# Optimization experiments

Measured on AMD Instinct MI355X. Metric: run time of the kernel, lower is better.

Reference implementation:

```python
import jax, jax.numpy as jnp
import numpy as np

B, T, C = 8, 512, 1024
H, E = 16, 64          # n_head, head_dim; H*E == C
L = 2048               # cached (prefix) length in the KV cache


def setup_inputs() -> dict:
    key = jax.random.key(0)
    ks = jax.random.split(key, 6)
    scale = 0.02
    return {
        "x": jax.random.normal(ks[0], (B, T, C), jnp.float32),
        "k_cache": jax.random.normal(ks[1], (B, H, L, E), jnp.float32),
        "v_cache": jax.random.normal(ks[2], (B, H, L, E), jnp.float32),
        "Wqkv": jax.random.normal(ks[3], (C, 3 * C), jnp.float32) * scale,
        "bqkv": jnp.zeros((3 * C,), jnp.float32),
        "Wproj": jax.random.normal(ks[4], (C, C), jnp.float32) * scale,
        "bproj": jnp.zeros((C,), jnp.float32),
    }


def reference(x, k_cache, v_cache, Wqkv, bqkv, Wproj, bproj):
    qkv = x @ Wqkv + bqkv
    q, k, v = jnp.split(qkv, 3, axis=-1)

    def to_heads(t):
        return t.reshape(B, T, H, E).transpose(0, 2, 1, 3)

    q, k, v = to_heads(q), to_heads(k), to_heads(v)

    # append new k,v to the cache (kv_cache.update + get)
    k_full = jnp.concatenate([k_cache, k], axis=2)  # (B,H,L+T,E)
    v_full = jnp.concatenate([v_cache, v], axis=2)

    # manual self-attention with cache-offset causal mask: row i (global pos L+i)
    # may attend to cols j <= L+i  (bias[L:L+T, :L+T])
    att = jnp.einsum("bhte,bhse->bhts", q, k_full) * (1.0 / np.sqrt(E))
    i = jnp.arange(T)[:, None] + L
    j = jnp.arange(L + T)[None, :]
    att = jnp.where(j <= i, att, -jnp.inf)
    att = jax.nn.softmax(att, axis=-1)

    y = jnp.einsum("bhts,bhse->bhte", att, v_full)
    y = y.transpose(0, 2, 1, 3).reshape(B, T, C)
    return y @ Wproj + bproj
```

## Files before the change

### kernel.cpp

```cpp
#include <hip/hip_runtime.h>
#include <hip/hip_bf16.h>

typedef unsigned short u16;
typedef unsigned int u32;

constexpr int B_ = 8, T_ = 512, C_ = 1024, H_ = 16, E_ = 64, L_ = 2048;
constexpr int S_ = L_ + T_;

typedef __bf16 bf16x8 __attribute__((ext_vector_type(8)));
typedef float f32x4 __attribute__((ext_vector_type(4)));

#define QSCALE 0.18033688011112042f

__device__ inline u16 f2bf(float f) {
  u32 u = __float_as_uint(f);
  u32 r = (u + 0x7fffu + ((u >> 16) & 1u)) >> 16;
  return (u16)r;
}

__device__ inline u32 pk2(float a, float b) {
  union { __hip_bfloat162 h; u32 u; } cv;
  cv.h = __float22bfloat162_rn(float2{a, b});
  return cv.u;
}

__device__ inline void gload_lds16(const u16* g, u16* l) {
  __builtin_amdgcn_global_load_lds(
      (const __attribute__((address_space(1))) u32*)g,
      (__attribute__((address_space(3))) u32*)l, 16, 0, 0);
}

__global__ __launch_bounds__(256) void convert_f32_bf16(const float* __restrict__ in,
                                                        u16* __restrict__ out) {
  const int i = blockIdx.x * 256 + threadIdx.x;
  const float4 a0 = ((const float4*)in)[i * 2];
  const float4 a1 = ((const float4*)in)[i * 2 + 1];
  uint4 p;
  p.x = pk2(a0.x, a0.y);
  p.y = pk2(a0.z, a0.w);
  p.z = pk2(a1.x, a1.y);
  p.w = pk2(a1.z, a1.w);
  ((uint4*)out)[i] = p;
}

__global__ __launch_bounds__(256) void transpose_f32_bf16(const float* __restrict__ in,
                                                          u16* __restrict__ out,
                                                          int R, int Ccols) {
  __shared__ u16 tile[64][65];
  const int r0 = blockIdx.y * 64;
  const int c0 = blockIdx.x * 64;
  const int tr = threadIdx.x >> 6;
  const int tc = threadIdx.x & 63;
#pragma unroll
  for (int i = 0; i < 16; ++i)
    tile[tr + i * 4][tc] = f2bf(in[(size_t)(r0 + tr + i * 4) * Ccols + c0 + tc]);
  __syncthreads();
#pragma unroll
  for (int i = 0; i < 16; ++i)
    out[(size_t)(c0 + tr + i * 4) * R + r0 + tc] = tile[tc][tr + i * 4];
}

__global__ __launch_bounds__(256) void prep_kv(const float* __restrict__ kc,
                                               const float* __restrict__ vc,
                                               u16* __restrict__ Km,
                                               u16* __restrict__ Vtm) {
  __shared__ u16 vt[64 * 72];
  const int s0 = (blockIdx.x & 31) * 64;
  const int bh = blockIdx.x >> 5;
  const int tid = threadIdx.x;
  const int srow = tid >> 2;
  const int eq = (tid & 3) * 16;

  {
    const float* kp = kc + ((size_t)bh * L_ + s0 + srow) * E_ + eq;
    float kv[16];
    *(float4*)(kv + 0) = *(const float4*)(kp + 0);
    *(float4*)(kv + 4) = *(const float4*)(kp + 4);
    *(float4*)(kv + 8) = *(const float4*)(kp + 8);
    *(float4*)(kv + 12) = *(const float4*)(kp + 12);
    uint4 p0, p1;
    p0.x = pk2(kv[0], kv[1]);
    p0.y = pk2(kv[2], kv[3]);
    p0.z = pk2(kv[4], kv[5]);
    p0.w = pk2(kv[6], kv[7]);
    p1.x = pk2(kv[8], kv[9]);
    p1.y = pk2(kv[10], kv[11]);
    p1.z = pk2(kv[12], kv[13]);
    p1.w = pk2(kv[14], kv[15]);
    u16* kd = Km + ((size_t)bh * S_ + s0 + srow) * E_ + eq;
    *(uint4*)kd = p0;
    *(uint4*)(kd + 8) = p1;
  }
  {
    const float* vp = vc + ((size_t)bh * L_ + s0 + srow) * E_ + eq;
    float vv[16];
    *(float4*)(vv + 0) = *(const float4*)(vp + 0);
    *(float4*)(vv + 4) = *(const float4*)(vp + 4);
    *(float4*)(vv + 8) = *(const float4*)(vp + 8);
    *(float4*)(vv + 12) = *(const float4*)(vp + 12);
    uint4 p0, p1;
    p0.x = pk2(vv[0], vv[1]);
    p0.y = pk2(vv[2], vv[3]);
    p0.z = pk2(vv[4], vv[5]);
    p0.w = pk2(vv[6], vv[7]);
    p1.x = pk2(vv[8], vv[9]);
    p1.y = pk2(vv[10], vv[11]);
    p1.z = pk2(vv[12], vv[13]);
    p1.w = pk2(vv[14], vv[15]);
    *(uint4*)(vt + srow * 72 + eq) = p0;
    *(uint4*)(vt + srow * 72 + eq + 8) = p1;
  }
  __syncthreads();
  {
    const int erow = tid >> 2;
    const int sq = (tid & 3) * 16;
    u16 o[16];
#pragma unroll
    for (int j = 0; j < 16; ++j) o[j] = vt[(sq + j) * 72 + erow];
    u16* vd = Vtm + ((size_t)bh * E_ + erow) * S_ + s0 + sq;
    *(uint4*)vd = *(uint4*)(o + 0);
    *(uint4*)(vd + 8) = *(uint4*)(o + 8);
  }
}

template <int MODE>
__global__ __launch_bounds__(256) void gemm128(const u16* __restrict__ A,
                                               const u16* __restrict__ BT,
                                               const float* __restrict__ bias,
                                               u16* __restrict__ qh,
                                               u16* __restrict__ Km,
                                               u16* __restrict__ Vtm,
                                               float* __restrict__ outf,
                                               int M, int N, int K) {
  __shared__ __align__(16) u16 As[128 * 32];
  __shared__ __align__(16) u16 Bs[128 * 32];
  const int tid = threadIdx.x;
  const int lane = tid & 63;
  const int w = tid >> 6;
  const int m0 = blockIdx.y * 128;
  const int n0 = blockIdx.x * 128;
  const int wm = (w >> 1) * 64;
  const int wn = (w & 1) * 64;
  const int fm = lane & 15;
  const int fk = (lane >> 4) * 8;

  const int srow = w * 16 + (lane >> 2);
  const int scol = (lane & 3) * 8;
  const u16* Ag = A + (size_t)(m0 + srow) * K + scol;
  const u16* Bg = BT + (size_t)(n0 + srow) * K + scol;
  u16* AsU = As + w * 512;
  u16* BsU = Bs + w * 512;

  f32x4 acc[4][4];
#pragma unroll
  for (int i = 0; i < 4; ++i)
#pragma unroll
    for (int j = 0; j < 4; ++j) acc[i][j] = f32x4{0.f, 0.f, 0.f, 0.f};

  for (int k0 = 0; k0 < K; k0 += 32) {
    gload_lds16(Ag, AsU);
    gload_lds16(Ag + (size_t)64 * K, AsU + 2048);
    gload_lds16(Bg, BsU);
    gload_lds16(Bg + (size_t)64 * K, BsU + 2048);
    Ag += 32;
    Bg += 32;
    __syncthreads();
    bf16x8 af[4], bf[4];
#pragma unroll
    for (int i = 0; i < 4; ++i)
      af[i] = *(const bf16x8*)(As + (wm + i * 16 + fm) * 32 + fk);
#pragma unroll
    for (int j = 0; j < 4; ++j)
      bf[j] = *(const bf16x8*)(Bs + (wn + j * 16 + fm) * 32 + fk);
#pragma unroll
    for (int i = 0; i < 4; ++i)
#pragma unroll
      for (int j = 0; j < 4; ++j)
        acc[i][j] = __builtin_amdgcn_mfma_f32_16x16x32_bf16(af[i], bf[j], acc[i][j], 0, 0, 0);
    __syncthreads();
  }

  const int rbase = (lane >> 4) * 4;
  const int cbase = lane & 15;
#pragma unroll
  for (int i = 0; i < 4; ++i)
#pragma unroll
    for (int j = 0; j < 4; ++j) {
      const int n = n0 + wn + j * 16 + cbase;
      const float bv = bias[n];
#pragma unroll
      for (int r = 0; r < 4; ++r) {
        const int m = m0 + wm + i * 16 + rbase + r;
        const float v = acc[i][j][r] + bv;
        if (MODE == 0) {
          const int seg = n >> 10;
          const int c = n & 1023;
          const int e = c & 63;
          const int bhh = ((m >> 9) * H_) + (c >> 6);
          const int t = m & 511;
          if (seg == 0)
            qh[((size_t)bhh * T_ + t) * E_ + e] = f2bf(v * QSCALE);
          else if (seg == 1)
            Km[((size_t)bhh * S_ + L_ + t) * E_ + e] = f2bf(v);
          else
            Vtm[((size_t)bhh * E_ + e) * S_ + L_ + t] = f2bf(v);
        } else {
          outf[(size_t)m * N + n] = v;
        }
      }
    }
}

__global__ __launch_bounds__(256) void attn_v3(const u16* __restrict__ qh,
                                               const u16* __restrict__ Km,
                                               const u16* __restrict__ Vtm,
                                               u16* __restrict__ y2) {
  __shared__ __align__(16) u16 Ks[64 * 72];
  __shared__ __align__(16) u16 Vts[64 * 72];
  __shared__ __align__(16) u16 Ps[4][32 * 72];

  const int tid = threadIdx.x;
  const int lane = tid & 63;
  const int w = tid >> 6;
  const int bh = blockIdx.x & 127;
  const int qt = blockIdx.x >> 7;
  const int h = bh & (H_ - 1);
  const int b = bh >> 4;
  const int t0 = qt * 128;

  const int col = lane & 15;
  const int fk = (lane >> 4) * 8;
  const int rbase = (lane >> 4) * 4;

  const u16* qbase = qh + ((size_t)bh * T_ + t0 + w * 32) * E_;
  bf16x8 qf[2][2];
#pragma unroll
  for (int q2 = 0; q2 < 2; ++q2)
#pragma unroll
    for (int ks = 0; ks < 2; ++ks)
      qf[q2][ks] = *(const bf16x8*)(qbase + (q2 * 16 + col) * E_ + ks * 32 + fk);

  const int srow = tid >> 2;
  const int sc8 = (tid & 3) * 16;

  f32x4 Yt[2][4];
  f32x4 lf[2];
#pragma unroll
  for (int q2 = 0; q2 < 2; ++q2) {
    lf[q2] = f32x4{0.f, 0.f, 0.f, 0.f};
#pragma unroll
    for (int et = 0; et < 4; ++et) Yt[q2][et] = f32x4{0.f, 0.f, 0.f, 0.f};
  }

  const bf16x8 ones = {(__bf16)1.f, (__bf16)1.f, (__bf16)1.f, (__bf16)1.f,
                       (__bf16)1.f, (__bf16)1.f, (__bf16)1.f, (__bf16)1.f};

  const int qmin_w = L_ + t0 + w * 32;
  const int nchunk = (L_ + t0 + 128) >> 6;
  const u16* KgB = Km + (size_t)bh * S_ * E_;
  const u16* VgB = Vtm + (size_t)bh * E_ * S_;

  for (int c0 = 0; c0 < nchunk; ++c0) {
    const int sbase = c0 << 6;
    __syncthreads();
    {
      const u16* kg = KgB + (size_t)(sbase + srow) * E_ + sc8;
      *(uint4*)(Ks + srow * 72 + sc8) = *(const uint4*)kg;
      *(uint4*)(Ks + srow * 72 + sc8 + 8) = *(const uint4*)(kg + 8);
      const u16* vg = VgB + (size_t)srow * S_ + sbase + sc8;
      *(uint4*)(Vts + srow * 72 + sc8) = *(const uint4*)vg;
      *(uint4*)(Vts + srow * 72 + sc8 + 8) = *(const uint4*)(vg + 8);
    }
    __syncthreads();

    if (sbase > qmin_w + 31) continue;

    f32x4 s[2][4];
#pragma unroll
    for (int kt = 0; kt < 4; ++kt) {
      const bf16x8 kb0 = *(const bf16x8*)(Ks + (kt * 16 + col) * 72 + fk);
      const bf16x8 kb1 = *(const bf16x8*)(Ks + (kt * 16 + col) * 72 + 32 + fk);
#pragma unroll
      for (int q2 = 0; q2 < 2; ++q2) {
        f32x4 z = {0.f, 0.f, 0.f, 0.f};
        z = __builtin_amdgcn_mfma_f32_16x16x32_bf16(qf[q2][0], kb0, z, 0, 0, 0);
        z = __builtin_amdgcn_mfma_f32_16x16x32_bf16(qf[q2][1], kb1, z, 0, 0, 0);
        s[q2][kt] = z;
      }
    }

    if (sbase + 63 > qmin_w) {
#pragma unroll
      for (int q2 = 0; q2 < 2; ++q2) {
        const int bound = qmin_w + q2 * 16 + rbase;
#pragma unroll
        for (int kt = 0; kt < 4; ++kt) {
          const int keypos = sbase + kt * 16 + col;
#pragma unroll
          for (int r = 0; r < 4; ++r)
            if (keypos > bound + r) s[q2][kt][r] = -1e30f;
        }
      }
    }

#pragma unroll
    for (int q2 = 0; q2 < 2; ++q2)
#pragma unroll
      for (int kt = 0; kt < 4; ++kt)
#pragma unroll
        for (int r = 0; r < 4; ++r) s[q2][kt][r] = exp2f(s[q2][kt][r]);

    u16* psw = Ps[w];
#pragma unroll
    for (int q2 = 0; q2 < 2; ++q2)
#pragma unroll
      for (int kt = 0; kt < 4; ++kt) {
        const u32 p01 = pk2(s[q2][kt][0], s[q2][kt][1]);
        const u32 p23 = pk2(s[q2][kt][2], s[q2][kt][3]);
        const int a = (q2 * 16 + rbase) * 72 + kt * 16 + col;
        psw[a] = (u16)p01;
        psw[a + 72] = (u16)(p01 >> 16);
        psw[a + 144] = (u16)p23;
        psw[a + 216] = (u16)(p23 >> 16);
      }

    bf16x8 pa[2][2];
#pragma unroll
    for (int q2 = 0; q2 < 2; ++q2)
#pragma unroll
      for (int ks = 0; ks < 2; ++ks)
        pa[q2][ks] = *(const bf16x8*)(psw + (q2 * 16 + col) * 72 + ks * 32 + fk);

#pragma unroll
    for (int q2 = 0; q2 < 2; ++q2) {
      lf[q2] = __builtin_amdgcn_mfma_f32_16x16x32_bf16(ones, pa[q2][0], lf[q2], 0, 0, 0);
      lf[q2] = __builtin_amdgcn_mfma_f32_16x16x32_bf16(ones, pa[q2][1], lf[q2], 0, 0, 0);
    }

#pragma unroll
    for (int et = 0; et < 4; ++et) {
      const bf16x8 vb0 = *(const bf16x8*)(Vts + (et * 16 + col) * 72 + fk);
      const bf16x8 vb1 = *(const bf16x8*)(Vts + (et * 16 + col) * 72 + 32 + fk);
#pragma unroll
      for (int q2 = 0; q2 < 2; ++q2) {
        Yt[q2][et] = __builtin_amdgcn_mfma_f32_16x16x32_bf16(vb0, pa[q2][0], Yt[q2][et], 0, 0, 0);
        Yt[q2][et] = __builtin_amdgcn_mfma_f32_16x16x32_bf16(vb1, pa[q2][1], Yt[q2][et], 0, 0, 0);
      }
    }
  }

#pragma unroll
  for (int q2 = 0; q2 < 2; ++q2) {
    const float rl = 1.f / lf[q2][0];
    const int t_out = t0 + w * 32 + q2 * 16 + col;
    u16* yp = y2 + ((size_t)b * T_ + t_out) * C_ + h * E_ + rbase;
#pragma unroll
    for (int et = 0; et < 4; ++et) {
      uint2 v;
      v.x = pk2(Yt[q2][et][0] * rl, Yt[q2][et][1] * rl);
      v.y = pk2(Yt[q2][et][2] * rl, Yt[q2][et][3] * rl);
      *(uint2*)(yp + et * 16) = v;
    }
  }
}

extern "C" void kernel_launch(void* const* d_in, const int* in_sizes, int n_in,
                              void* d_out, int out_size, void* d_ws, size_t ws_size,
                              hipStream_t stream) {
  const float* x = (const float*)d_in[0];
  const float* kc = (const float*)d_in[1];
  const float* vc = (const float*)d_in[2];
  const float* Wqkv = (const float*)d_in[3];
  const float* bqkv = (const float*)d_in[4];
  const float* Wproj = (const float*)d_in[5];
  const float* bproj = (const float*)d_in[6];
  float* out = (float*)d_out;

  u16* qh = (u16*)d_ws;
  u16* y2 = qh + 4194304;
  u16* xb = y2 + 4194304;
  u16* WqT = xb + 4194304;
  u16* WpT = WqT + 3145728;
  u16* Km = WpT + 1048576;
  u16* Vtm = Km + 20971520;

  convert_f32_bf16<<<dim3(2048), 256, 0, stream>>>(x, xb);
  transpose_f32_bf16<<<dim3(48, 16), 256, 0, stream>>>(Wqkv, WqT, 1024, 3072);
  transpose_f32_bf16<<<dim3(16, 16), 256, 0, stream>>>(Wproj, WpT, 1024, 1024);
  prep_kv<<<dim3(128 * 32), 256, 0, stream>>>(kc, vc, Km, Vtm);

  gemm128<0><<<dim3(24, 32), 256, 0, stream>>>(xb, WqT, bqkv, qh, Km, Vtm, nullptr,
                                               4096, 3072, 1024);

  attn_v3<<<dim3(512), 256, 0, stream>>>(qh, Km, Vtm, y2);

  gemm128<1><<<dim3(8, 32), 256, 0, stream>>>(y2, WpT, bproj, nullptr, nullptr,
                                              nullptr, out, 4096, 1024, 1024);
}
```

Before: 356.0 us.

## Rewrite attention with 32x32 MFMA, register P via permlane, double-buffered swizzled LDS

The attention kernel now uses 32x32x16 bf16 MFMA tiles, computing S^T so the softmax probabilities can be repacked into the PV operand in registers with v_permlane32_swap. This removes the per-wave P round trip through LDS. K/V tiles are double-buffered, with global loads for the next chunk issued into registers before compute, and stored into an XOR-swizzled unpadded LDS layout. Launch bounds now request 2 blocks per CU. The risks are higher register pressure from the f32x16 accumulators and correctness depending on the permlane layout.

```diff
diff --git a/kernel.cpp b/kernel.cpp
--- a/kernel.cpp
+++ b/kernel.cpp
@@ -9,6 +9,7 @@
 
 typedef __bf16 bf16x8 __attribute__((ext_vector_type(8)));
 typedef float f32x4 __attribute__((ext_vector_type(4)));
+typedef float f32x16 __attribute__((ext_vector_type(16)));
 
 #define QSCALE 0.18033688011112042f
 
@@ -22,6 +23,10 @@
   union { __hip_bfloat162 h; u32 u; } cv;
   cv.h = __float22bfloat162_rn(float2{a, b});
   return cv.u;
+}
+
+__device__ inline void pl32swap(u32& a, u32& b) {
+  asm("v_permlane32_swap_b32 %0, %1" : "+v"(a), "+v"(b));
 }
 
 __device__ inline void gload_lds16(const u16* g, u16* l) {
@@ -211,13 +216,12 @@
     }
 }
 
-__global__ __launch_bounds__(256) void attn_v3(const u16* __restrict__ qh,
-                                               const u16* __restrict__ Km,
-                                               const u16* __restrict__ Vtm,
-                                               u16* __restrict__ y2) {
-  __shared__ __align__(16) u16 Ks[64 * 72];
-  __shared__ __align__(16) u16 Vts[64 * 72];
-  __shared__ __align__(16) u16 Ps[4][32 * 72];
+__global__ __launch_bounds__(256, 2) void attn_v4(const u16* __restrict__ qh,
+                                                  const u16* __restrict__ Km,
+                                                  const u16* __restrict__ Vtm,
+                                                  u16* __restrict__ y2) {
+  __shared__ __align__(16) u16 Ks[2][64 * 64];
+  __shared__ __align__(16) u16 Vts[2][64 * 64];
 
   const int tid = threadIdx.x;
   const int lane = tid & 63;
@@ -228,28 +232,29 @@
   const int b = bh >> 4;
   const int t0 = qt * 128;
 
-  const int col = lane & 15;
-  const int fk = (lane >> 4) * 8;
-  const int rbase = (lane >> 4) * 4;
-
-  const u16* qbase = qh + ((size_t)bh * T_ + t0 + w * 32) * E_;
-  bf16x8 qf[2][2];
-#pragma unroll
-  for (int q2 = 0; q2 < 2; ++q2)
-#pragma unroll
-    for (int ks = 0; ks < 2; ++ks)
-      qf[q2][ks] = *(const bf16x8*)(qbase + (q2 * 16 + col) * E_ + ks * 32 + fk);
+  const int ln = lane & 31;
+  const int hi = lane >> 5;
+  const int swz = ln & 7;
+
+  const u16* qbase = qh + ((size_t)bh * T_ + t0 + w * 32 + ln) * E_;
+  bf16x8 qf[4];
+#pragma unroll
+  for (int et = 0; et < 4; ++et)
+    qf[et] = *(const bf16x8*)(qbase + et * 16 + hi * 8);
 
   const int srow = tid >> 2;
-  const int sc8 = (tid & 3) * 16;
-
-  f32x4 Yt[2][4];
-  f32x4 lf[2];
-#pragma unroll
-  for (int q2 = 0; q2 < 2; ++q2) {
-    lf[q2] = f32x4{0.f, 0.f, 0.f, 0.f};
-#pragma unroll
-    for (int et = 0; et < 4; ++et) Yt[q2][et] = f32x4{0.f, 0.f, 0.f, 0.f};
+  const int su = (tid & 3) * 2;
+  const u16* kg = Km + ((size_t)bh * S_ + srow) * E_ + su * 8;
+  const u16* vg = Vtm + ((size_t)bh * E_ + srow) * S_ + su * 8;
+  const int st0 = srow * 64 + ((su ^ (srow & 7)) * 8);
+  const int st1 = srow * 64 + (((su + 1) ^ (srow & 7)) * 8);
+
+  f32x16 Yt[2], lacc;
+#pragma unroll
+  for (int i = 0; i < 16; ++i) {
+    Yt[0][i] = 0.f;
+    Yt[1][i] = 0.f;
+    lacc[i] = 0.f;
   }
 
   const bf16x8 ones = {(__bf16)1.f, (__bf16)1.f, (__bf16)1.f, (__bf16)1.f,
@@ -257,111 +262,117 @@
 
   const int qmin_w = L_ + t0 + w * 32;
   const int nchunk = (L_ + t0 + 128) >> 6;
-  const u16* KgB = Km + (size_t)bh * S_ * E_;
-  const u16* VgB = Vtm + (size_t)bh * E_ * S_;
-
-  for (int c0 = 0; c0 < nchunk; ++c0) {
-    const int sbase = c0 << 6;
-    __syncthreads();
-    {
-      const u16* kg = KgB + (size_t)(sbase + srow) * E_ + sc8;
-      *(uint4*)(Ks + srow * 72 + sc8) = *(const uint4*)kg;
-      *(uint4*)(Ks + srow * 72 + sc8 + 8) = *(const uint4*)(kg + 8);
-      const u16* vg = VgB + (size_t)srow * S_ + sbase + sc8;
-      *(uint4*)(Vts + srow * 72 + sc8) = *(const uint4*)vg;
-      *(uint4*)(Vts + srow * 72 + sc8 + 8) = *(const uint4*)(vg + 8);
+
+  uint4 kr0 = *(const uint4*)(kg);
+  uint4 kr1 = *(const uint4*)(kg + 8);
+  uint4 vr0 = *(const uint4*)(vg);
+  uint4 vr1 = *(const uint4*)(vg + 8);
+  {
+    u16* kd = Ks[0];
+    u16* vd = Vts[0];
+    *(uint4*)(kd + st0) = kr0;
+    *(uint4*)(kd + st1) = kr1;
+    *(uint4*)(vd + st0) = vr0;
+    *(uint4*)(vd + st1) = vr1;
+  }
+  __syncthreads();
+
+  for (int c = 0; c < nchunk; ++c) {
+    const int sbase = c << 6;
+    const u16* ks = Ks[c & 1];
+    const u16* vs = Vts[c & 1];
+    const bool more = (c + 1 < nchunk);
+
+    if (more) {
+      const size_t ko = (size_t)(c + 1) * 64 * E_;
+      const int vo = (c + 1) * 64;
+      kr0 = *(const uint4*)(kg + ko);
+      kr1 = *(const uint4*)(kg + ko + 8);
+      vr0 = *(const uint4*)(vg + vo);
+      vr1 = *(const uint4*)(vg + vo + 8);
+    }
+
+    if (sbase <= qmin_w + 31) {
+      bf16x8 pa[4];
+#pragma unroll
+      for (int kb = 0; kb < 2; ++kb) {
+        f32x16 s;
+#pragma unroll
+        for (int i = 0; i < 16; ++i) s[i] = 0.f;
+#pragma unroll
+        for (int et = 0; et < 4; ++et) {
+          const bf16x8 kf = *(const bf16x8*)(
+              ks + (kb * 32 + ln) * 64 + (((et * 2 + hi) ^ swz) * 8));
+          s = __builtin_amdgcn_mfma_f32_32x32x16_bf16(kf, qf[et], s, 0, 0, 0);
+        }
+
+        if (sbase + 63 > qmin_w) {
+          const int qpos = qmin_w + ln;
+          const int kb0 = sbase + kb * 32 + hi * 4;
+#pragma unroll
+          for (int r = 0; r < 16; ++r) {
+            const int keypos = kb0 + (r & 3) + 8 * (r >> 2);
+            if (keypos > qpos) s[r] = -1e30f;
+          }
+        }
+
+#pragma unroll
+        for (int r = 0; r < 16; ++r) s[r] = exp2f(s[r]);
+
+#pragma unroll
+        for (int t = 0; t < 2; ++t) {
+          u32 x0 = pk2(s[8 * t + 0], s[8 * t + 1]);
+          u32 y0 = pk2(s[8 * t + 4], s[8 * t + 5]);
+          u32 x1 = pk2(s[8 * t + 2], s[8 * t + 3]);
+          u32 y1 = pk2(s[8 * t + 6], s[8 * t + 7]);
+          pl32swap(x0, y0);
+          pl32swap(x1, y1);
+          union { u32 u[4]; bf16x8 v; } pu;
+          pu.u[0] = x0;
+          pu.u[1] = x1;
+          pu.u[2] = y0;
+          pu.u[3] = y1;
+          pa[kb * 2 + t] = pu.v;
+        }
+      }
+
+#pragma unroll
+      for (int t = 0; t < 4; ++t)
+        lacc = __builtin_amdgcn_mfma_f32_32x32x16_bf16(ones, pa[t], lacc, 0, 0, 0);
+
+#pragma unroll
+      for (int eb = 0; eb < 2; ++eb)
+#pragma unroll
+        for (int t = 0; t < 4; ++t) {
+          const bf16x8 vf = *(const bf16x8*)(
+              vs + (eb * 32 + ln) * 64 + (((t * 2 + hi) ^ swz) * 8));
+          Yt[eb] = __builtin_amdgcn_mfma_f32_32x32x16_bf16(vf, pa[t], Yt[eb], 0, 0, 0);
+        }
+    }
+
+    if (more) {
+      u16* kd = Ks[(c + 1) & 1];
+      u16* vd = Vts[(c + 1) & 1];
+      *(uint4*)(kd + st0) = kr0;
+      *(uint4*)(kd + st1) = kr1;
+      *(uint4*)(vd + st0) = vr0;
+      *(uint4*)(vd + st1) = vr1;
     }
     __syncthreads();
-
-    if (sbase > qmin_w + 31) continue;
-
-    f32x4 s[2][4];
-#pragma unroll
-    for (int kt = 0; kt < 4; ++kt) {
-      const bf16x8 kb0 = *(const bf16x8*)(Ks + (kt * 16 + col) * 72 + fk);
-      const bf16x8 kb1 = *(const bf16x8*)(Ks + (kt * 16 + col) * 72 + 32 + fk);
-#pragma unroll
-      for (int q2 = 0; q2 < 2; ++q2) {
-        f32x4 z = {0.f, 0.f, 0.f, 0.f};
-        z = __builtin_amdgcn_mfma_f32_16x16x32_bf16(qf[q2][0], kb0, z, 0, 0, 0);
-        z = __builtin_amdgcn_mfma_f32_16x16x32_bf16(qf[q2][1], kb1, z, 0, 0, 0);
-        s[q2][kt] = z;
-      }
+  }
+
+  const float rl = 1.f / lacc[0];
+  const int t_out = t0 + w * 32 + ln;
+  u16* yp = y2 + ((size_t)b * T_ + t_out) * C_ + h * E_ + hi * 4;
+#pragma unroll
+  for (int eb = 0; eb < 2; ++eb)
+#pragma unroll
+    for (int g = 0; g < 4; ++g) {
+      uint2 st;
+      st.x = pk2(Yt[eb][4 * g + 0] * rl, Yt[eb][4 * g + 1] * rl);
+      st.y = pk2(Yt[eb][4 * g + 2] * rl, Yt[eb][4 * g + 3] * rl);
+      *(uint2*)(yp + eb * 32 + g * 8) = st;
     }
-
-    if (sbase + 63 > qmin_w) {
-#pragma unroll
-      for (int q2 = 0; q2 < 2; ++q2) {
-        const int bound = qmin_w + q2 * 16 + rbase;
-#pragma unroll
-        for (int kt = 0; kt < 4; ++kt) {
-          const int keypos = sbase + kt * 16 + col;
-#pragma unroll
-          for (int r = 0; r < 4; ++r)
-            if (keypos > bound + r) s[q2][kt][r] = -1e30f;
-        }
-      }
-    }
-
-#pragma unroll
-    for (int q2 = 0; q2 < 2; ++q2)
-#pragma unroll
-      for (int kt = 0; kt < 4; ++kt)
-#pragma unroll
-        for (int r = 0; r < 4; ++r) s[q2][kt][r] = exp2f(s[q2][kt][r]);
-
-    u16* psw = Ps[w];
-#pragma unroll
-    for (int q2 = 0; q2 < 2; ++q2)
-#pragma unroll
-      for (int kt = 0; kt < 4; ++kt) {
-        const u32 p01 = pk2(s[q2][kt][0], s[q2][kt][1]);
-        const u32 p23 = pk2(s[q2][kt][2], s[q2][kt][3]);
-        const int a = (q2 * 16 + rbase) * 72 + kt * 16 + col;
-        psw[a] = (u16)p01;
-        psw[a + 72] = (u16)(p01 >> 16);
-        psw[a + 144] = (u16)p23;
-        psw[a + 216] = (u16)(p23 >> 16);
-      }
-
-    bf16x8 pa[2][2];
-#pragma unroll
-    for (int q2 = 0; q2 < 2; ++q2)
-#pragma unroll
-      for (int ks = 0; ks < 2; ++ks)
-        pa[q2][ks] = *(const bf16x8*)(psw + (q2 * 16 + col) * 72 + ks * 32 + fk);
-
-#pragma unroll
-    for (int q2 = 0; q2 < 2; ++q2) {
-      lf[q2] = __builtin_amdgcn_mfma_f32_16x16x32_bf16(ones, pa[q2][0], lf[q2], 0, 0, 0);
-      lf[q2] = __builtin_amdgcn_mfma_f32_16x16x32_bf16(ones, pa[q2][1], lf[q2], 0, 0, 0);
-    }
-
-#pragma unroll
-    for (int et = 0; et < 4; ++et) {
-      const bf16x8 vb0 = *(const bf16x8*)(Vts + (et * 16 + col) * 72 + fk);
-      const bf16x8 vb1 = *(const bf16x8*)(Vts + (et * 16 + col) * 72 + 32 + fk);
-#pragma unroll
-      for (int q2 = 0; q2 < 2; ++q2) {
-        Yt[q2][et] = __builtin_amdgcn_mfma_f32_16x16x32_bf16(vb0, pa[q2][0], Yt[q2][et], 0, 0, 0);
-        Yt[q2][et] = __builtin_amdgcn_mfma_f32_16x16x32_bf16(vb1, pa[q2][1], Yt[q2][et], 0, 0, 0);
-      }
-    }
-  }
-
-#pragma unroll
-  for (int q2 = 0; q2 < 2; ++q2) {
-    const float rl = 1.f / lf[q2][0];
-    const int t_out = t0 + w * 32 + q2 * 16 + col;
-    u16* yp = y2 + ((size_t)b * T_ + t_out) * C_ + h * E_ + rbase;
-#pragma unroll
-    for (int et = 0; et < 4; ++et) {
-      uint2 v;
-      v.x = pk2(Yt[q2][et][0] * rl, Yt[q2][et][1] * rl);
-      v.y = pk2(Yt[q2][et][2] * rl, Yt[q2][et][3] * rl);
-      *(uint2*)(yp + et * 16) = v;
-    }
-  }
 }
 
 extern "C" void kernel_launch(void* const* d_in, const int* in_sizes, int n_in,
@@ -392,7 +403,7 @@
   gemm128<0><<<dim3(24, 32), 256, 0, stream>>>(xb, WqT, bqkv, qh, Km, Vtm, nullptr,
                                                4096, 3072, 1024);
 
-  attn_v3<<<dim3(512), 256, 0, stream>>>(qh, Km, Vtm, y2);
+  attn_v4<<<dim3(512), 256, 0, stream>>>(qh, Km, Vtm, y2);
 
   gemm128<1><<<dim3(8, 32), 256, 0, stream>>>(y2, WpT, bproj, nullptr, nullptr,
                                               nullptr, out, 4096, 1024, 1024);
```

Result: faster. 343.6 us (-3.5%).
